# Kernel tuning notes

Hardware: AMD Instinct MI355X
Metric: run time of the kernel (lower is better)

## Reference

```python
import jax, jax.numpy as jnp
import numpy as np


def _chamfer(xyz1, xyz2):
    # xyz1: [B, N, 3], xyz2: [B, M, 3]
    sq1 = jnp.sum(xyz1 * xyz1, axis=-1)            # [B, N]
    sq2 = jnp.sum(xyz2 * xyz2, axis=-1)            # [B, M]
    inner = jnp.einsum('bnd,bmd->bnm', xyz1, xyz2) # [B, N, M]
    d = sq1[:, :, None] + sq2[:, None, :] - 2.0 * inner
    d = jnp.maximum(d, 0.0)  # guard tiny negatives from cancellation
    dist1 = jnp.min(d, axis=2)  # [B, N] nearest in xyz2 for each point of xyz1
    dist2 = jnp.min(d, axis=1)  # [B, M]
    return jnp.mean(dist1) + jnp.mean(dist2)


def setup_inputs() -> dict:
    key = jax.random.key(0)
    k1, k2 = jax.random.split(key)
    B, N, M = 16, 4096, 4096
    xyz1 = jax.random.normal(k1, (B, N, 3), dtype=jnp.float32)
    xyz2 = jax.random.normal(k2, (B, M, 3), dtype=jnp.float32)
    return {"xyz1": xyz1, "xyz2": xyz2}


def reference(xyz1, xyz2):
    return _chamfer(xyz1, xyz2)
```

## Files before the change

### kernel.cpp

```cpp
#include <hip/hip_runtime.h>


#define BATCH 16
#define NPTS  4096
#define NQ_TOTAL (BATCH * NPTS)

typedef __attribute__((ext_vector_type(8)))  short bf16x8;
typedef __attribute__((ext_vector_type(16))) float f32x16;
typedef __attribute__((ext_vector_type(4)))  unsigned int u32x4;

union FragCast { bf16x8 v; u32x4 u; };

__device__ __forceinline__ unsigned short bf16_rne(float v) {
    unsigned u = __float_as_uint(v);
    u += 0x7FFFu + ((u >> 16) & 1u);
    return (unsigned short)(u >> 16);
}
__device__ __forceinline__ float bf16f(unsigned short h) {
    return __uint_as_float(((unsigned)h) << 16);
}

__global__ __launch_bounds__(256, 2) void chamfer_fused_kernel(
    const float* __restrict__ xyz1, const float* __restrict__ xyz2,
    float* __restrict__ partials)
{
    const int orig = (int)blockIdx.x;
    const int wfid = (orig & 7) * 64 + (orig >> 3);
    const int og = wfid & 15;
    const int b  = (wfid >> 4) & 15;
    const int d  = wfid >> 8;

    const int tid = (int)threadIdx.x;
    const int wid = tid >> 6;
    const int l   = tid & 63;
    const int c   = l & 31;
    const int g   = l >> 5;
    const int strip0 = og * 8 + wid;
    const int strip1 = og * 8 + wid + 4;

    const float* qpts = d ? xyz2 : xyz1;
    const float* tpts = d ? xyz1 : xyz2;

    const unsigned short one = 0x3F80;
    bf16x8 af0, af1;
    #pragma unroll
    for (int s = 0; s < 2; ++s) {
        const int strip = s ? strip1 : strip0;
        const int qi = b * NPTS + strip * 32 + c;
        const float qx = qpts[qi * 3 + 0];
        const float qy = qpts[qi * 3 + 1];
        const float qz = qpts[qi * 3 + 2];
        const float mx = -2.0f * qx, my = -2.0f * qy, mz = -2.0f * qz;
        const float Q  = fmaf(qx, qx, fmaf(qy, qy, qz * qz));
        const unsigned short xh = bf16_rne(mx), xl = bf16_rne(mx - bf16f(xh));
        const unsigned short yh = bf16_rne(my), yl = bf16_rne(my - bf16f(yh));
        const unsigned short zh = bf16_rne(mz), zl = bf16_rne(mz - bf16f(zh));
        const unsigned short Qh = bf16_rne(Q),  Ql = bf16_rne(Q - bf16f(Qh));
        bf16x8 af;
        if (g == 0) {
            af[0] = (short)xh; af[1] = (short)xh; af[2] = (short)xl; af[3] = (short)yh;
            af[4] = (short)yh; af[5] = (short)yl; af[6] = (short)zh; af[7] = (short)zh;
        } else {
            af[0] = (short)zl; af[1] = (short)one; af[2] = (short)one; af[3] = (short)Qh;
            af[4] = (short)Ql; af[5] = 0;          af[6] = 0;          af[7] = 0;
        }
        if (s) af1 = af; else af0 = af;
    }

    f32x16 vzero;
    #pragma unroll
    for (int i = 0; i < 16; ++i) vzero[i] = 0.0f;

    f32x16 rm0, rm1;
    #pragma unroll
    for (int i = 0; i < 16; ++i) { rm0[i] = 1e30f; rm1[i] = 1e30f; }

    __shared__ u32x4 lds[64 * 64];

    for (int cc = 0; cc < 2; ++cc) {
        __syncthreads();

        const float* tb = tpts + ((size_t)b * NPTS + (size_t)cc * 2048) * 3;
        #pragma unroll
        for (int k = 0; k < 8; ++k) {
            const int pi = k * 256 + tid;
            const float x = tb[pi * 3 + 0];
            const float y = tb[pi * 3 + 1];
            const float z = tb[pi * 3 + 2];
            const float S = fmaf(x, x, fmaf(y, y, z * z));
            const unsigned short Xh = bf16_rne(x), Xl = bf16_rne(x - bf16f(Xh));
            const unsigned short Yh = bf16_rne(y), Yl = bf16_rne(y - bf16f(Yh));
            const unsigned short Zh = bf16_rne(z), Zl = bf16_rne(z - bf16f(Zh));
            const unsigned short Sh = bf16_rne(S), Sl = bf16_rne(S - bf16f(Sh));
            FragCast f0, f1;
            f0.v[0] = (short)Xh; f0.v[1] = (short)Xl; f0.v[2] = (short)Xh; f0.v[3] = (short)Yh;
            f0.v[4] = (short)Yl; f0.v[5] = (short)Yh; f0.v[6] = (short)Zh; f0.v[7] = (short)Zl;
            f1.v[0] = (short)Zh; f1.v[1] = (short)Sh; f1.v[2] = (short)Sl; f1.v[3] = (short)one;
            f1.v[4] = (short)one; f1.v[5] = 0;        f1.v[6] = 0;         f1.v[7] = 0;
            const int t  = pi >> 5;
            const int c2 = pi & 31;
            lds[t * 64 + c2]      = f0.u;
            lds[t * 64 + 32 + c2] = f1.u;
        }
        __syncthreads();

        #pragma unroll 2
        for (int t = 0; t < 64; t += 2) {
            FragCast ta, tb2;
            ta.u  = lds[(t + 0) * 64 + l];
            tb2.u = lds[(t + 1) * 64 + l];
            f32x16 a0 = __builtin_amdgcn_mfma_f32_32x32x16_bf16(af0, ta.v,  vzero, 0, 0, 0);
            f32x16 a1 = __builtin_amdgcn_mfma_f32_32x32x16_bf16(af0, tb2.v, vzero, 0, 0, 0);
            f32x16 b0 = __builtin_amdgcn_mfma_f32_32x32x16_bf16(af1, ta.v,  vzero, 0, 0, 0);
            f32x16 b1 = __builtin_amdgcn_mfma_f32_32x32x16_bf16(af1, tb2.v, vzero, 0, 0, 0);
            #pragma unroll
            for (int i = 0; i < 16; ++i) {
                rm0[i] = fminf(fminf(rm0[i], a0[i]), a1[i]);
                rm1[i] = fminf(fminf(rm1[i], b0[i]), b1[i]);
            }
        }
    }

    #pragma unroll
    for (int m = 1; m <= 16; m <<= 1) {
        #pragma unroll
        for (int i = 0; i < 16; ++i) {
            rm0[i] = fminf(rm0[i], __shfl_xor(rm0[i], m, 64));
            rm1[i] = fminf(rm1[i], __shfl_xor(rm1[i], m, 64));
        }
    }

    float s0 = 0.0f, s1 = 0.0f;
    #pragma unroll
    for (int i = 0; i < 16; ++i) {
        s0 += fmaxf(rm0[i], 0.0f);
        s1 += fmaxf(rm1[i], 0.0f);
    }
    s0 += __shfl_xor(s0, 32, 64);
    s1 += __shfl_xor(s1, 32, 64);
    const float s = s0 + s1;

    __shared__ float wsum[4];
    if (l == 0) wsum[wid] = s;
    __syncthreads();
    if (tid == 0)
        partials[orig] = wsum[0] + wsum[1] + wsum[2] + wsum[3];
}

__global__ __launch_bounds__(256) void final_kernel(
    const float* __restrict__ partials, float* __restrict__ out)
{
    const int t = (int)threadIdx.x;
    float v = partials[t] + partials[t + 256];

    #pragma unroll
    for (int off = 32; off >= 1; off >>= 1)
        v += __shfl_down(v, off, 64);

    __shared__ float wsum[4];
    const int lane = t & 63;
    const int wid  = t >> 6;
    if (lane == 0) wsum[wid] = v;
    __syncthreads();
    if (t == 0)
        out[0] = (wsum[0] + wsum[1] + wsum[2] + wsum[3]) * (1.0f / (float)NQ_TOTAL);
}

extern "C" void kernel_launch(void* const* d_in, const int* in_sizes, int n_in,
                              void* d_out, int out_size, void* d_ws, size_t ws_size,
                              hipStream_t stream) {
    const float* xyz1 = (const float*)d_in[0];
    const float* xyz2 = (const float*)d_in[1];
    float* out = (float*)d_out;
    float* partials = (float*)d_ws;

    chamfer_fused_kernel<<<512, 256, 0, stream>>>(xyz1, xyz2, partials);
    final_kernel<<<1, 256, 0, stream>>>(partials, out);
}
```

Baseline: 27.08 us.

## Split target dimension across two blocks and combine row minima in extra kernel

New measurement: 47.04 us. +73.7%, slower.

```diff
diff --git a/kernel.cpp b/kernel.cpp
--- a/kernel.cpp
+++ b/kernel.cpp
@@ -20,20 +20,21 @@
     return __uint_as_float(((unsigned)h) << 16);
 }
 
-__global__ __launch_bounds__(256, 2) void chamfer_fused_kernel(
+__global__ __launch_bounds__(256, 2) void chamfer_main_kernel(
     const float* __restrict__ xyz1, const float* __restrict__ xyz2,
-    float* __restrict__ partials)
+    float* __restrict__ rowmin)
 {
     const int orig = (int)blockIdx.x;
-    const int wfid = (orig & 7) * 64 + (orig >> 3);
-    const int og = wfid & 15;
-    const int b  = (wfid >> 4) & 15;
-    const int d  = wfid >> 8;
+    const int wfid = (orig & 7) * 128 + (orig >> 3);
+    const int h  = wfid & 1;
+    const int og = (wfid >> 1) & 15;
+    const int b  = (wfid >> 5) & 15;
+    const int d  = wfid >> 9;
 
     const int tid = (int)threadIdx.x;
     const int wid = tid >> 6;
     const int l   = tid & 63;
-    const int c   = l & 31;
+    const int lc  = l & 31;
     const int g   = l >> 5;
     const int strip0 = og * 8 + wid;
     const int strip1 = og * 8 + wid + 4;
@@ -46,7 +47,7 @@
     #pragma unroll
     for (int s = 0; s < 2; ++s) {
         const int strip = s ? strip1 : strip0;
-        const int qi = b * NPTS + strip * 32 + c;
+        const int qi = b * NPTS + strip * 32 + lc;
         const float qx = qpts[qi * 3 + 0];
         const float qy = qpts[qi * 3 + 1];
         const float qz = qpts[qi * 3 + 2];
@@ -75,14 +76,16 @@
     #pragma unroll
     for (int i = 0; i < 16; ++i) { rm0[i] = 1e30f; rm1[i] = 1e30f; }
 
-    __shared__ u32x4 lds[64 * 64];
+    __shared__ u32x4 lds[32 * 64];
+
+    const float* tptr = tpts + (size_t)b * NPTS * 3;
 
     for (int cc = 0; cc < 2; ++cc) {
         __syncthreads();
 
-        const float* tb = tpts + ((size_t)b * NPTS + (size_t)cc * 2048) * 3;
+        const float* tb = tptr + ((size_t)h * 2048 + (size_t)cc * 1024) * 3;
         #pragma unroll
-        for (int k = 0; k < 8; ++k) {
+        for (int k = 0; k < 4; ++k) {
             const int pi = k * 256 + tid;
             const float x = tb[pi * 3 + 0];
             const float y = tb[pi * 3 + 1];
@@ -105,7 +108,7 @@
         __syncthreads();
 
         #pragma unroll 2
-        for (int t = 0; t < 64; t += 2) {
+        for (int t = 0; t < 32; t += 2) {
             FragCast ta, tb2;
             ta.u  = lds[(t + 0) * 64 + l];
             tb2.u = lds[(t + 1) * 64 + l];
@@ -115,8 +118,8 @@
             f32x16 b1 = __builtin_amdgcn_mfma_f32_32x32x16_bf16(af1, tb2.v, vzero, 0, 0, 0);
             #pragma unroll
             for (int i = 0; i < 16; ++i) {
-                rm0[i] = fminf(fminf(rm0[i], a0[i]), a1[i]);
-                rm1[i] = fminf(fminf(rm1[i], b0[i]), b1[i]);
+                rm0[i] = fminf(rm0[i], fminf(a0[i], a1[i]));
+                rm1[i] = fminf(rm1[i], fminf(b0[i], b1[i]));
             }
         }
     }
@@ -130,21 +133,38 @@
         }
     }
 
-    float s0 = 0.0f, s1 = 0.0f;
-    #pragma unroll
-    for (int i = 0; i < 16; ++i) {
-        s0 += fmaxf(rm0[i], 0.0f);
-        s1 += fmaxf(rm1[i], 0.0f);
-    }
-    s0 += __shfl_xor(s0, 32, 64);
-    s1 += __shfl_xor(s1, 32, 64);
-    const float s = s0 + s1;
+    if (lc == 0) {
+        const size_t base = ((size_t)(((d * 16 + b) * 16 + og) * 2 + h)) * 256;
+        #pragma unroll
+        for (int i = 0; i < 16; ++i) {
+            const int row = (i & 3) + 8 * (i >> 2) + 4 * g;
+            rowmin[base + (size_t)wid * 32 + row]       = rm0[i];
+            rowmin[base + (size_t)(wid + 4) * 32 + row] = rm1[i];
+        }
+    }
+}
+
+__global__ __launch_bounds__(256) void combine_kernel(
+    const float* __restrict__ rowmin, float* __restrict__ partials)
+{
+    const int p = (int)blockIdx.x;
+    const int j = (int)threadIdx.x;
+
+    const float a = rowmin[((size_t)p * 2 + 0) * 256 + j];
+    const float b = rowmin[((size_t)p * 2 + 1) * 256 + j];
+    float v = fmaxf(fminf(a, b), 0.0f) * (1.0f / (float)NQ_TOTAL);
+
+    #pragma unroll
+    for (int off = 32; off >= 1; off >>= 1)
+        v += __shfl_down(v, off, 64);
 
     __shared__ float wsum[4];
-    if (l == 0) wsum[wid] = s;
+    const int lane = j & 63;
+    const int wid  = j >> 6;
+    if (lane == 0) wsum[wid] = v;
     __syncthreads();
-    if (tid == 0)
-        partials[orig] = wsum[0] + wsum[1] + wsum[2] + wsum[3];
+    if (j == 0)
+        partials[p] = wsum[0] + wsum[1] + wsum[2] + wsum[3];
 }
 
 __global__ __launch_bounds__(256) void final_kernel(
@@ -163,7 +183,7 @@
     if (lane == 0) wsum[wid] = v;
     __syncthreads();
     if (t == 0)
-        out[0] = (wsum[0] + wsum[1] + wsum[2] + wsum[3]) * (1.0f / (float)NQ_TOTAL);
+        out[0] = wsum[0] + wsum[1] + wsum[2] + wsum[3];
 }
 
 extern "C" void kernel_launch(void* const* d_in, const int* in_sizes, int n_in,
@@ -172,8 +192,11 @@
     const float* xyz1 = (const float*)d_in[0];
     const float* xyz2 = (const float*)d_in[1];
     float* out = (float*)d_out;
-    float* partials = (float*)d_ws;
-
-    chamfer_fused_kernel<<<512, 256, 0, stream>>>(xyz1, xyz2, partials);
+
+    float* rowmin   = (float*)d_ws;
+    float* partials = (float*)d_ws + 512 * 2 * 256;
+
+    chamfer_main_kernel<<<1024, 256, 0, stream>>>(xyz1, xyz2, rowmin);
+    combine_kernel<<<512, 256, 0, stream>>>(rowmin, partials);
     final_kernel<<<1, 256, 0, stream>>>(partials, out);
 }
```
